# Optimization experiments

Measured on AMD Instinct MI355X. Metric: run time of the kernel, lower is better.

Reference implementation:

```python
import jax, jax.numpy as jnp
import numpy as np

SHIFT = 7  # shift_size; pad = 3


def _gn(x, w, b, eps=1e-5):
    # GroupNorm(1, C): normalize over (C,H,W) per sample, affine per channel
    m = jnp.mean(x, axis=(1, 2, 3), keepdims=True)
    v = jnp.var(x, axis=(1, 2, 3), keepdims=True)
    return (x - m) * jax.lax.rsqrt(v + eps) * w[None, :, None, None] + b[None, :, None, None]


def _conv1x1(x, w, b):
    return jnp.einsum('bchw,oc->bohw', x, w) + b[None, :, None, None]


def _gelu(x):
    return jax.nn.gelu(x, approximate=False)


def _shift_h(x, size):
    # CUDA kernel semantics: g = c // ceil(C/size); s = -(g - size//2);
    # out[n,c,h,w] = x[n,c,h+s,w] if in-bounds else 0  (dim=2)
    B, C, H, W = x.shape
    pad = size // 2
    group = -(-C // size)  # ceil
    s = pad - (jnp.arange(C) // group)              # [C], values in [-pad, pad]
    xp = jnp.pad(x, ((0, 0), (0, 0), (pad, pad), (0, 0)))
    idx = jnp.arange(H)[None, :] + s[:, None] + pad  # [C,H], in [0, H+2p-1]
    c = jnp.arange(C)[:, None]
    return xp[:, c, idx, :]


def _shift_w(x, size):
    return _shift_h(x.swapaxes(2, 3), size).swapaxes(2, 3)


def _axial_shift(x, c1w, c1b, n1w, n1b, c21w, c21b, c22w, c22b, n2w, n2b, c3w, c3b):
    x = _gelu(_gn(_conv1x1(x, c1w, c1b), n1w, n1b))
    x_lr = _shift_w(x, SHIFT)
    x_td = _shift_h(x, SHIFT)
    x_lr = _gelu(_conv1x1(x_lr, c21w, c21b))
    x_td = _gelu(_conv1x1(x_td, c22w, c22b))
    x = _gn(x_lr + x_td, n2w, n2b)
    return _conv1x1(x, c3w, c3b)


def setup_inputs() -> dict:
    B, C, H, W = 16, 256, 56, 56
    HID = 4 * C
    key = jax.random.key(0)
    ks = jax.random.split(key, 8)
    wscale = 0.05
    inp = {
        'x': jax.random.normal(ks[0], (B, C, H, W), jnp.float32),
        'n1_w': jnp.ones((C,), jnp.float32), 'n1_b': jnp.zeros((C,), jnp.float32),
        'as_c1_w': jax.random.normal(ks[1], (C, C), jnp.float32) * wscale,
        'as_c1_b': jnp.zeros((C,), jnp.float32),
        'as_n1_w': jnp.ones((C,), jnp.float32), 'as_n1_b': jnp.zeros((C,), jnp.float32),
        'as_c21_w': jax.random.normal(ks[2], (C, C), jnp.float32) * wscale,
        'as_c21_b': jnp.zeros((C,), jnp.float32),
        'as_c22_w': jax.random.normal(ks[3], (C, C), jnp.float32) * wscale,
        'as_c22_b': jnp.zeros((C,), jnp.float32),
        'as_n2_w': jnp.ones((C,), jnp.float32), 'as_n2_b': jnp.zeros((C,), jnp.float32),
        'as_c3_w': jax.random.normal(ks[4], (C, C), jnp.float32) * wscale,
        'as_c3_b': jnp.zeros((C,), jnp.float32),
        'n2_w': jnp.ones((C,), jnp.float32), 'n2_b': jnp.zeros((C,), jnp.float32),
        'fc1_w': jax.random.normal(ks[5], (HID, C), jnp.float32) * wscale,
        'fc1_b': jnp.zeros((HID,), jnp.float32),
        'fc2_w': jax.random.normal(ks[6], (C, HID), jnp.float32) * wscale,
        'fc2_b': jnp.zeros((C,), jnp.float32),
    }
    return inp


def reference(x, n1_w, n1_b, as_c1_w, as_c1_b, as_n1_w, as_n1_b,
              as_c21_w, as_c21_b, as_c22_w, as_c22_b, as_n2_w, as_n2_b,
              as_c3_w, as_c3_b, n2_w, n2_b, fc1_w, fc1_b, fc2_w, fc2_b):
    # AxialShiftedBlock: x = x + AxialShift(norm1(x)); x = x + Mlp(norm2(x))
    h = _gn(x, n1_w, n1_b)
    h = _axial_shift(h, as_c1_w, as_c1_b, as_n1_w, as_n1_b,
                     as_c21_w, as_c21_b, as_c22_w, as_c22_b,
                     as_n2_w, as_n2_b, as_c3_w, as_c3_b)
    x = x + h
    h = _gn(x, n2_w, n2_b)
    h = _gelu(_conv1x1(h, fc1_w, fc1_b))
    h = _conv1x1(h, fc2_w, fc2_b)
    return x + h
```

## Files before the change

kernel.cpp:

```cpp
#include <hip/hip_runtime.h>

typedef __attribute__((ext_vector_type(4))) float f32x4;
typedef __attribute__((ext_vector_type(8))) short bf16x8;
typedef __attribute__((ext_vector_type(4))) unsigned short u16x4;
typedef unsigned short u16;

#define HW 3136
#define NSEG 49
#define NELF 802816.0f
#define EPS 1e-5f

__device__ __forceinline__ short f2bf(float f) {
  union { float f; unsigned u; } v; v.f = f;
  unsigned r = (v.u + 0x7FFFu + ((v.u >> 16) & 1u)) >> 16;
  return (short)r;
}
__device__ __forceinline__ float b2f(u16 u) {
  union { unsigned u; float f; } v; v.u = ((unsigned)u) << 16;
  return v.f;
}
__device__ __forceinline__ float fgelu(float x) {
  float x2 = x * x;
  float u = x * (0.7978845608f + 0.0356774081f * x2);
  float e = __expf(-2.0f * u);
  return x * __builtin_amdgcn_rcpf(1.0f + e);
}
__device__ __forceinline__ void gload16(const void* g, void* l) {
  __builtin_amdgcn_global_load_lds(
      (const __attribute__((address_space(1))) void*)(uintptr_t)g,
      (__attribute__((address_space(3))) void*)(unsigned)(uintptr_t)l,
      16, 0, 0);
}

__global__ void wfold_kernel(const float* __restrict__ c1, const float* __restrict__ c21,
                             const float* __restrict__ c22, const float* __restrict__ c3,
                             const float* __restrict__ fc1, const float* __restrict__ fc2,
                             const float* __restrict__ n1w, const float* __restrict__ an2w,
                             const float* __restrict__ n2w, u16* __restrict__ out) {
  int i = (blockIdx.x * 256 + threadIdx.x) * 4;
  const float* src; int off; const float* scale = nullptr;
  if (i < 65536)       { src = c1;  off = 0;       scale = n1w; }
  else if (i < 131072) { src = c21; off = 65536; }
  else if (i < 196608) { src = c22; off = 131072; }
  else if (i < 262144) { src = c3;  off = 196608;  scale = an2w; }
  else if (i < 524288) { src = fc1; off = 262144;  scale = n2w; }
  else                 { src = fc2; off = 524288; }
  int li = i - off;
  float4 v = *(const float4*)(src + li);
  if (scale) {
    float4 g = *(const float4*)(scale + (li & 255));
    v.x *= g.x; v.y *= g.y; v.z *= g.z; v.w *= g.w;
  }
  u16x4 o4; o4[0] = (u16)f2bf(v.x); o4[1] = (u16)f2bf(v.y); o4[2] = (u16)f2bf(v.z); o4[3] = (u16)f2bf(v.w);
  *(u16x4*)(out + i) = o4;
}

__global__ void rowsum_kernel(const float* __restrict__ c1w, const float* __restrict__ c1b,
                              const float* __restrict__ n1w, const float* __restrict__ n1b,
                              const float* __restrict__ c3w, const float* __restrict__ c3b,
                              const float* __restrict__ an2w, const float* __restrict__ an2b,
                              const float* __restrict__ fc1w, const float* __restrict__ fc1b,
                              const float* __restrict__ n2w, const float* __restrict__ n2b,
                              float* __restrict__ sums) {
  int o = blockIdx.x * 256 + threadIdx.x;
  const float *W, *gw, *gb, *cb; float *Sg, *Sb; int row;
  if (o < 256)      { W = c1w;  gw = n1w;  gb = n1b;  cb = c1b;  Sg = sums;        Sb = sums + 256;  row = o; }
  else if (o < 512) { W = c3w;  gw = an2w; gb = an2b; cb = c3b;  Sg = sums + 512;  Sb = sums + 768;  row = o - 256; }
  else              { W = fc1w; gw = n2w;  gb = n2b;  cb = fc1b; Sg = sums + 1024; Sb = sums + 2048; row = o - 512; }
  float sg = 0.f, sb = 0.f;
  for (int c = 0; c < 256; c += 4) {
    float4 w = *(const float4*)(W + (size_t)row * 256 + c);
    float4 g = *(const float4*)(gw + c);
    float4 b = *(const float4*)(gb + c);
    sg += w.x * g.x + w.y * g.y + w.z * g.z + w.w * g.w;
    sb += w.x * b.x + w.y * b.y + w.z * b.z + w.w * b.w;
  }
  Sg[row] = sg; Sb[row] = sb + cb[row];
}

__global__ __launch_bounds__(256) void t0_kernel(const float* __restrict__ x,
                                                 u16* __restrict__ xT, float* __restrict__ st) {
  __shared__ __align__(16) u16 tile[64 * 256];
  const int t = threadIdx.x;
  const int n = blockIdx.x / NSEG;
  const int hw0 = (blockIdx.x % NSEG) * 64;
  const int pix = t & 63;
  float s = 0.f, q = 0.f;
#pragma unroll
  for (int r = 0; r < 16; ++r) {
    int cq = (t >> 6) + (r << 2);
    int c = cq * 4;
    u16x4 o4;
#pragma unroll
    for (int i = 0; i < 4; ++i) {
      float v = x[((size_t)n * 256 + c + i) * HW + hw0 + pix];
      s += v; q += v * v;
      o4[i] = (u16)f2bf(v);
    }
    int u = cq ^ ((pix & 15) << 2);
    *(u16x4*)((char*)tile + pix * 512 + u * 8) = o4;
  }
  __syncthreads();
  {
    const int p2 = t >> 2;
#pragma unroll
    for (int r = 0; r < 8; ++r) {
      int oct = (t & 3) + (r << 2);
      int up = (2 * oct) ^ ((p2 & 15) << 2);
      bf16x8 v = *(const bf16x8*)((char*)tile + p2 * 512 + up * 8);
      *(bf16x8*)&xT[((size_t)n * HW + hw0 + p2) * 256 + oct * 8] = v;
    }
  }
  __syncthreads();
  float* red = (float*)tile;
  red[t] = s; red[256 + t] = q;
  __syncthreads();
  for (int off = 128; off > 0; off >>= 1) {
    if (t < off) { red[t] += red[t + off]; red[256 + t] += red[256 + t + off]; }
    __syncthreads();
  }
  if (t == 0) { atomicAdd(&st[n * 2], red[0]); atomicAdd(&st[n * 2 + 1], red[256]); }
}

__global__ void e2_kernel(const u16* __restrict__ y, u16* __restrict__ tb,
                          const float* __restrict__ gw, const float* __restrict__ gb,
                          const float* __restrict__ stats) {
  const size_t NG = (size_t)16 * HW * 32;
  for (size_t g = (size_t)blockIdx.x * blockDim.x + threadIdx.x; g < NG;
       g += (size_t)gridDim.x * blockDim.x) {
    size_t base = g * 8;
    int n = (int)(base / 802816);
    int c0 = (int)(base & 255);
    float sm = stats[n * 2], sq = stats[n * 2 + 1];
    float mn = sm * (1.0f / NELF);
    float rstd = rsqrtf(sq * (1.0f / NELF) - mn * mn + EPS);
    bf16x8 v = *(const bf16x8*)(y + base);
    bf16x8 o;
#pragma unroll
    for (int j = 0; j < 8; ++j) {
      float sc = rstd * gw[c0 + j];
      float sh = gb[c0 + j] - mn * sc;
      o[j] = f2bf(fgelu(b2f((u16)v[j]) * sc + sh));
    }
    *(bf16x8*)(tb + base) = o;
  }
}

template<int EPI>
__global__ __launch_bounds__(512, 2) void gemmW2(
    const u16* __restrict__ actT, const u16* __restrict__ wt,
    const float* __restrict__ Sg, const float* __restrict__ Sb,
    const float* __restrict__ stats_in, float* __restrict__ stats_out,
    const u16* __restrict__ residCL, u16* __restrict__ outT)
{
  __shared__ __align__(16) u16 lds[79872];
  const int t = threadIdx.x;
  const int lane = t & 63, wave = t >> 6;
  const int fr = lane & 15, fq = lane >> 4;
  const int wo = wave >> 1, wp = wave & 1;
  const int n = blockIdx.x / 14;
  const int hw0 = (blockIdx.x % 14) * 224;
  const size_t nHW = (size_t)n * HW;

  {
    int u0 = t, u1 = t + 512;
    int r0 = u0 >> 2, sg0 = ((u0 & 3) - (r0 >> 1)) & 3;
    int r1 = u1 >> 2, sg1 = ((u1 & 3) - (r1 >> 1)) & 3;
    const u16* w0 = wt + (size_t)r0 * 256 + sg0 * 8;
    const u16* w1 = wt + (size_t)r1 * 256 + sg1 * 8;
#pragma unroll
    for (int k = 0; k < 8; ++k) {
      gload16(w0 + k * 32, &lds[k * 8192 + wave * 512]);
      gload16(w1 + k * 32, &lds[k * 8192 + 4096 + wave * 512]);
    }
  }

  int aU[4];
#pragma unroll
  for (int os = 0; os < 4; ++os) { int row = wo * 64 + os * 16 + fr; aU[os] = (4 * row + ((fq + (row >> 1)) & 3)) * 8; }
  int bO[7];
#pragma unroll
  for (int ps = 0; ps < 7; ++ps) {
    int pix = wp * 112 + ps * 16 + fr;
    bO[ps] = (pix * 4 + (fq ^ (pix & 3))) * 8;
  }

  const u16* srcB0; const u16* srcB1;
  {
    int v0 = wave * 128 + lane, v1 = v0 + 64;
    int p0 = v0 >> 2, j0 = (v0 & 3) ^ (p0 & 3);
    int p1 = v1 >> 2, j1 = (v1 & 3) ^ (p1 & 3);
    srcB0 = actT + (nHW + hw0 + p0) * 256 + j0 * 8;
    srcB1 = actT + (nHW + hw0 + p1) * 256 + j1 * 8;
  }
  auto stageB = [&](int par, int ks) {
    if (wave < 7) {
      gload16(srcB0 + ks * 32, &lds[65536 + par * 7168 + (wave * 128) * 8]);
      gload16(srcB1 + ks * 32, &lds[65536 + par * 7168 + (wave * 128 + 64) * 8]);
    }
  };

  f32x4 acc[4][7];
#pragma unroll
  for (int a = 0; a < 4; ++a)
#pragma unroll
    for (int b = 0; b < 7; ++b) acc[a][b] = (f32x4){0.f, 0.f, 0.f, 0.f};

  stageB(0, 0);
  __syncthreads();

#pragma unroll
  for (int k = 0; k < 8; ++k) {
    if (k < 7) stageB((k + 1) & 1, k + 1);
    bf16x8 afr[4], bfr[7];
#pragma unroll
    for (int os = 0; os < 4; ++os) afr[os] = *(const bf16x8*)&lds[k * 8192 + aU[os]];
#pragma unroll
    for (int ps = 0; ps < 7; ++ps) bfr[ps] = *(const bf16x8*)&lds[65536 + (k & 1) * 7168 + bO[ps]];
#pragma unroll
    for (int os = 0; os < 4; ++os)
#pragma unroll
      for (int ps = 0; ps < 7; ++ps)
        acc[os][ps] = __builtin_amdgcn_mfma_f32_16x16x32_bf16(afr[os], bfr[ps], acc[os][ps], 0, 0, 0);
    __syncthreads();
  }

  char* tl = (char*)lds;
  float sm = stats_in[n * 2], sq = stats_in[n * 2 + 1];
  float mn = sm * (1.0f / NELF);
  float rstd = rsqrtf(sq * (1.0f / NELF) - mn * mn + EPS);
  float mr = mn * rstd;
  float lsum = 0.f, lsq = 0.f;
#pragma unroll
  for (int os = 0; os < 4; ++os) {
    const int ob = wo * 64 + os * 16 + fq * 4;
    float4 g4 = *(const float4*)&Sg[ob];
    float4 s4 = *(const float4*)&Sb[ob];
    float be[4] = {s4.x - mr * g4.x, s4.y - mr * g4.y, s4.z - mr * g4.z, s4.w - mr * g4.w};
#pragma unroll
    for (int ps = 0; ps < 7; ++ps) {
      const int pix = wp * 112 + ps * 16 + fr;
      u16x4 rv = {0, 0, 0, 0};
      if (EPI == 1) rv = *(const u16x4*)&residCL[(nHW + hw0 + pix) * 256 + ob];
      u16x4 pk;
#pragma unroll
      for (int j = 0; j < 4; ++j) {
        float v = fmaf(acc[os][ps][j], rstd, be[j]);
        if (EPI == 1) v += b2f(rv[j]);
        lsum += v; lsq += v * v;
        pk[j] = (u16)f2bf(v);
      }
      const int qd = wo * 16 + os * 4 + fq;
      const int uq = qd ^ ((pix & 15) << 2);
      *(u16x4*)(tl + pix * 512 + uq * 8) = pk;
    }
  }
  __syncthreads();
#pragma unroll
  for (int r = 0; r < 14; ++r) {
    int idx = t + r * 512;
    int pix = idx >> 5, oct = idx & 31;
    int up = (2 * oct) ^ ((pix & 15) << 2);
    bf16x8 v = *(const bf16x8*)(tl + pix * 512 + up * 8);
    *(bf16x8*)&outT[(nHW + hw0 + pix) * 256 + oct * 8] = v;
  }
  __syncthreads();
  float* red = (float*)lds;
  red[t] = lsum; red[512 + t] = lsq;
  __syncthreads();
  for (int off = 256; off > 0; off >>= 1) {
    if (t < off) { red[t] += red[t + off]; red[512 + t] += red[512 + t + off]; }
    __syncthreads();
  }
  if (t == 0) { atomicAdd(&stats_out[n * 2], red[0]); atomicAdd(&stats_out[n * 2 + 1], red[512]); }
}

__global__ __launch_bounds__(512, 2) void gemm_dual4(
    const u16* __restrict__ tT, const u16* __restrict__ w21, const u16* __restrict__ w22,
    const float* __restrict__ b21, const float* __restrict__ b22,
    float* __restrict__ stats_out, u16* __restrict__ zT)
{
  __shared__ __align__(16) u16 lds[47616];
  const int t = threadIdx.x;
  const int lane = t & 63, wave = t >> 6;
  const int fr = lane & 15, fq = lane >> 4;
  const int n = blockIdx.x / 28;
  const int hw0 = (blockIdx.x % 28) * 112;
  const size_t nHW = (size_t)n * HW;

  const int u = (t < 448) ? t : 447;
  const int jl = u / 112, p = u - jl * 112;
  const int pix = hw0 + p;
  const int wc = pix % 56, hc = pix / 56;

  bf16x8 gA0, gA1, gB0, gB1;
  auto gatherIssue = [&](int ks) {
    int c0 = ks * 32 + jl * 8;
    int g0 = c0 / 37;
    int s0 = 3 - g0;
    int pa0 = pix + s0;           pa0 = pa0 < 0 ? 0 : (pa0 > HW - 1 ? HW - 1 : pa0);
    int pa1 = pix + s0 - 1;       pa1 = pa1 < 0 ? 0 : (pa1 > HW - 1 ? HW - 1 : pa1);
    int pb0 = pix + 56 * s0;      pb0 = pb0 < 0 ? 0 : (pb0 > HW - 1 ? HW - 1 : pb0);
    int pb1 = pix + 56 * (s0 - 1); pb1 = pb1 < 0 ? 0 : (pb1 > HW - 1 ? HW - 1 : pb1);
    gA0 = *(const bf16x8*)(tT + (nHW + pa0) * 256 + c0);
    gA1 = *(const bf16x8*)(tT + (nHW + pa1) * 256 + c0);
    gB0 = *(const bf16x8*)(tT + (nHW + pb0) * 256 + c0);
    gB1 = *(const bf16x8*)(tT + (nHW + pb1) * 256 + c0);
  };
  auto gatherWrite = [&](int par, int ks) {
    int c0 = ks * 32 + jl * 8;
    int g0 = c0 / 37;
    int s0 = 3 - g0;
    int js = (g0 + 1) * 37 - c0; if (js > 8) js = 8;
    bool a0 = (unsigned)(wc + s0) < 56u, a1 = (unsigned)(wc + s0 - 1) < 56u;
    bool b0 = (unsigned)(hc + s0) < 56u, b1 = (unsigned)(hc + s0 - 1) < 56u;
    bf16x8 va, vb;
#pragma unroll
    for (int j = 0; j < 8; ++j) {
      bool lo = j < js;
      va[j] = lo ? (a0 ? gA0[j] : (short)0) : (a1 ? gA1[j] : (short)0);
      vb[j] = lo ? (b0 ? gB0[j] : (short)0) : (b1 ? gB1[j] : (short)0);
    }
    if (t < 448) {
      *(bf16x8*)&lds[32768 + par * 3712 + (jl * 116 + p) * 8] = va;
      *(bf16x8*)&lds[40192 + par * 3712 + (jl * 116 + p) * 8] = vb;
    }
  };
  auto stageW = [&](int par, int ks) {
    int u0 = t; int r0 = u0 >> 2, sg0 = ((u0 & 3) - (r0 >> 1)) & 3;
    int u1 = t + 512; int r1 = u1 >> 2, sg1 = ((u1 & 3) - (r1 >> 1)) & 3;
    gload16(w21 + (size_t)r0 * 256 + ks * 32 + sg0 * 8, &lds[par * 8192 + wave * 512]);
    gload16(w21 + (size_t)r1 * 256 + ks * 32 + sg1 * 8, &lds[par * 8192 + 4096 + wave * 512]);
    gload16(w22 + (size_t)r0 * 256 + ks * 32 + sg0 * 8, &lds[16384 + par * 8192 + wave * 512]);
    gload16(w22 + (size_t)r1 * 256 + ks * 32 + sg1 * 8, &lds[16384 + par * 8192 + 4096 + wave * 512]);
  };

  int aU[2], bP[7];
#pragma unroll
  for (int os = 0; os < 2; ++os) { int row = wave * 32 + os * 16 + fr; aU[os] = (4 * row + ((fq + (row >> 1)) & 3)) * 8; }
#pragma unroll
  for (int ps = 0; ps < 7; ++ps) bP[ps] = (fq * 116 + ps * 16 + fr) * 8;

  f32x4 accA[2][7], accB[2][7];
#pragma unroll
  for (int a = 0; a < 2; ++a)
#pragma unroll
    for (int b = 0; b < 7; ++b) { accA[a][b] = (f32x4){0, 0, 0, 0}; accB[a][b] = (f32x4){0, 0, 0, 0}; }

  gatherIssue(0);
  stageW(0, 0);
  gatherWrite(0, 0);
  gatherIssue(1);
  __syncthreads();

#pragma unroll
  for (int k = 0; k < 8; ++k) {
    if (k < 7) stageW((k + 1) & 1, k + 1);
    bf16x8 afA[2], afB[2], bfA[7], bfB[7];
#pragma unroll
    for (int os = 0; os < 2; ++os) {
      afA[os] = *(const bf16x8*)&lds[(k & 1) * 8192 + aU[os]];
      afB[os] = *(const bf16x8*)&lds[16384 + (k & 1) * 8192 + aU[os]];
    }
#pragma unroll
    for (int ps = 0; ps < 7; ++ps) {
      bfA[ps] = *(const bf16x8*)&lds[32768 + (k & 1) * 3712 + bP[ps]];
      bfB[ps] = *(const bf16x8*)&lds[40192 + (k & 1) * 3712 + bP[ps]];
    }
#pragma unroll
    for (int os = 0; os < 2; ++os)
#pragma unroll
      for (int ps = 0; ps < 7; ++ps) {
        accA[os][ps] = __builtin_amdgcn_mfma_f32_16x16x32_bf16(afA[os], bfA[ps], accA[os][ps], 0, 0, 0);
        accB[os][ps] = __builtin_amdgcn_mfma_f32_16x16x32_bf16(afB[os], bfB[ps], accB[os][ps], 0, 0, 0);
      }
    if (k < 7) {
      gatherWrite((k + 1) & 1, k + 1);
      if (k < 6) gatherIssue(k + 2);
    }
    __syncthreads();
  }

  char* tl = (char*)lds;
  float lsum = 0.f, lsq = 0.f;
#pragma unroll
  for (int os = 0; os < 2; ++os) {
    const int ob = wave * 32 + os * 16 + fq * 4;
    float4 a4 = *(const float4*)&b21[ob];
    float4 c4 = *(const float4*)&b22[ob];
    float ba[4] = {a4.x, a4.y, a4.z, a4.w};
    float bb[4] = {c4.x, c4.y, c4.z, c4.w};
#pragma unroll
    for (int ps = 0; ps < 7; ++ps) {
      const int pixL = ps * 16 + fr;
      u16x4 pk;
#pragma unroll
      for (int j = 0; j < 4; ++j) {
        float z = fgelu(accA[os][ps][j] + ba[j]) + fgelu(accB[os][ps][j] + bb[j]);
        lsum += z; lsq += z * z;
        pk[j] = (u16)f2bf(z);
      }
      const int qd = wave * 8 + os * 4 + fq;
      const int uq = qd ^ ((pixL & 15) << 2);
      *(u16x4*)(tl + pixL * 512 + uq * 8) = pk;
    }
  }
  __syncthreads();
#pragma unroll
  for (int r = 0; r < 7; ++r) {
    int idx = t + r * 512;
    int pixL = idx >> 5, oct = idx & 31;
    int up = (2 * oct) ^ ((pixL & 15) << 2);
    bf16x8 v = *(const bf16x8*)(tl + pixL * 512 + up * 8);
    *(bf16x8*)&zT[(nHW + hw0 + pixL) * 256 + oct * 8] = v;
  }
  __syncthreads();
  float* red = (float*)lds;
  red[t] = lsum; red[512 + t] = lsq;
  __syncthreads();
  for (int off = 256; off > 0; off >>= 1) {
    if (t < off) { red[t] += red[t + off]; red[512 + t] += red[512 + t + off]; }
    __syncthreads();
  }
  if (t == 0) { atomicAdd(&stats_out[n * 2], red[0]); atomicAdd(&stats_out[n * 2 + 1], red[512]); }
}

__global__ __launch_bounds__(512, 2) void gemm_mlp(
    const u16* __restrict__ x2T, const u16* __restrict__ wfc1, const u16* __restrict__ wfc2,
    const float* __restrict__ Sg, const float* __restrict__ Sb, const float* __restrict__ bias2,
    const float* __restrict__ stats_in, float* __restrict__ out_f32)
{
  __shared__ __align__(16) u16 lds[75008];
  const int t = threadIdx.x;
  const int lane = t & 63, wave = t >> 6;
  const int fr = lane & 15, fq = lane >> 4;
  const int n = blockIdx.x / 28;
  const int hw0 = (blockIdx.x % 28) * 112;
  const size_t nHW = (size_t)n * HW;

  auto stageWm = [&](int par, int s) {
    int chunk = s >> 4, kk = s & 7;
    int u0 = t; int r0 = u0 >> 2, sg0 = ((u0 & 3) - (r0 >> 1)) & 3;
    int u1 = t + 512; int r1 = u1 >> 2, sg1 = ((u1 & 3) - (r1 >> 1)) & 3;
    if (((s >> 3) & 1) == 0) {
      gload16(wfc1 + (size_t)(chunk * 256 + r0) * 256 + kk * 32 + sg0 * 8, &lds[par * 8192 + wave * 512]);
      gload16(wfc1 + (size_t)(chunk * 256 + r1) * 256 + kk * 32 + sg1 * 8, &lds[par * 8192 + 4096 + wave * 512]);
    } else {
      gload16(wfc2 + (size_t)r0 * 1024 + chunk * 256 + kk * 32 + sg0 * 8, &lds[par * 8192 + wave * 512]);
      gload16(wfc2 + (size_t)r1 * 1024 + chunk * 256 + kk * 32 + sg1 * 8, &lds[par * 8192 + 4096 + wave * 512]);
    }
  };

#pragma unroll
  for (int i = 0; i < 7; ++i) {
    int u = wave * 448 + i * 64 + lane;
    int j = u / 112, p = u - j * 112;
    bf16x8 v = *(const bf16x8*)(x2T + (nHW + hw0 + p) * 256 + j * 8);
    *(bf16x8*)&lds[16384 + (j * 113 + p) * 8] = v;
  }
  stageWm(0, 0);

  float sm = stats_in[n * 2], sq = stats_in[n * 2 + 1];
  float mn = sm * (1.0f / NELF);
  float rstd = rsqrtf(sq * (1.0f / NELF) - mn * mn + EPS);
  float mr = mn * rstd;

  int aU[2];
#pragma unroll
  for (int os = 0; os < 2; ++os) { int row = wave * 32 + os * 16 + fr; aU[os] = (4 * row + ((fq + (row >> 1)) & 3)) * 8; }

  f32x4 hacc[2][7], oacc[2][7];
#pragma unroll
  for (int a = 0; a < 2; ++a)
#pragma unroll
    for (int b = 0; b < 7; ++b) { hacc[a][b] = (f32x4){0, 0, 0, 0}; oacc[a][b] = (f32x4){0, 0, 0, 0}; }

  __syncthreads();

  for (int s = 0; s < 64; ++s) {
    if (s < 63) stageWm((s + 1) & 1, s + 1);
    const int kk = s & 7;
    const bool bph = (s >> 3) & 1;
    bf16x8 afr[2], bfr[7];
#pragma unroll
    for (int os = 0; os < 2; ++os) afr[os] = *(const bf16x8*)&lds[(s & 1) * 8192 + aU[os]];
    if (!bph) {
#pragma unroll
      for (int ps = 0; ps < 7; ++ps)
        bfr[ps] = *(const bf16x8*)&lds[16384 + ((kk * 4 + fq) * 113 + ps * 16 + fr) * 8];
#pragma unroll
      for (int os = 0; os < 2; ++os)
#pragma unroll
        for (int ps = 0; ps < 7; ++ps)
          hacc[os][ps] = __builtin_amdgcn_mfma_f32_16x16x32_bf16(afr[os], bfr[ps], hacc[os][ps], 0, 0, 0);
    } else {
#pragma unroll
      for (int ps = 0; ps < 7; ++ps)
        bfr[ps] = *(const bf16x8*)&lds[45312 + ((kk * 4 + fq) * 116 + ps * 16 + fr) * 8];
#pragma unroll
      for (int os = 0; os < 2; ++os)
#pragma unroll
        for (int ps = 0; ps < 7; ++ps)
          oacc[os][ps] = __builtin_amdgcn_mfma_f32_16x16x32_bf16(afr[os], bfr[ps], oacc[os][ps], 0, 0, 0);
    }
    if ((s & 15) == 7) {
      const int hcb = (s >> 4) * 256;
#pragma unroll
      for (int os = 0; os < 2; ++os) {
        const int hcl = wave * 32 + os * 16 + fq * 4;
        const int hc = hcb + hcl;
        float4 g4 = *(const float4*)&Sg[hc];
        float4 s4 = *(const float4*)&Sb[hc];
        float be[4] = {s4.x - mr * g4.x, s4.y - mr * g4.y, s4.z - mr * g4.z, s4.w - mr * g4.w};
        const int jH = hcl >> 3;
#pragma unroll
        for (int ps = 0; ps < 7; ++ps) {
          const int pixL = ps * 16 + fr;
          u16x4 pk;
#pragma unroll
          for (int j = 0; j < 4; ++j)
            pk[j] = (u16)f2bf(fgelu(fmaf(hacc[os][ps][j], rstd, be[j])));
          *(u16x4*)&lds[45312 + (jH * 116 + pixL) * 8 + (fq & 1) * 4] = pk;
          hacc[os][ps] = (f32x4){0, 0, 0, 0};
        }
      }
    }
    __syncthreads();
  }

#pragma unroll
  for (int os = 0; os < 2; ++os) {
    const int ob = wave * 32 + os * 16 + fq * 4;
    float4 b4 = *(const float4*)&bias2[ob];
    float bb[4] = {b4.x, b4.y, b4.z, b4.w};
#pragma unroll
    for (int ps = 0; ps < 7; ++ps) {
      const int pixL = ps * 16 + fr;
      u16x4 rv = *(const u16x4*)&lds[16384 + ((ob >> 3) * 113 + pixL) * 8 + (ob & 4)];
#pragma unroll
      for (int j = 0; j < 4; ++j) {
        float v = oacc[os][ps][j] + bb[j] + b2f(rv[j]);
        out_f32[((size_t)n * 256 + ob + j) * HW + hw0 + pixL] = v;
      }
    }
  }
}

extern "C" void kernel_launch(void* const* d_in, const int* in_sizes, int n_in,
                              void* d_out, int out_size, void* d_ws, size_t ws_size,
                              hipStream_t stream) {
  const float* x     = (const float*)d_in[0];
  const float* n1_w  = (const float*)d_in[1];
  const float* n1_b  = (const float*)d_in[2];
  const float* c1_w  = (const float*)d_in[3];
  const float* c1_b  = (const float*)d_in[4];
  const float* an1_w = (const float*)d_in[5];
  const float* an1_b = (const float*)d_in[6];
  const float* c21_w = (const float*)d_in[7];
  const float* c21_b = (const float*)d_in[8];
  const float* c22_w = (const float*)d_in[9];
  const float* c22_b = (const float*)d_in[10];
  const float* an2_w = (const float*)d_in[11];
  const float* an2_b = (const float*)d_in[12];
  const float* c3_w  = (const float*)d_in[13];
  const float* c3_b  = (const float*)d_in[14];
  const float* n2_w  = (const float*)d_in[15];
  const float* n2_b  = (const float*)d_in[16];
  const float* fc1_w = (const float*)d_in[17];
  const float* fc1_b = (const float*)d_in[18];
  const float* fc2_w = (const float*)d_in[19];
  const float* fc2_b = (const float*)d_in[20];

  char* ws = (char*)d_ws;
  float* stats = (float*)ws;
  float* sums  = (float*)(ws + 1024);
  u16* wbuf = (u16*)(ws + 16384);
  u16* wb_c1g  = wbuf;
  u16* wb_c21  = wbuf + 65536;
  u16* wb_c22  = wbuf + 131072;
  u16* wb_c3g  = wbuf + 196608;
  u16* wb_fc1g = wbuf + 262144;
  u16* wb_fc2  = wbuf + 524288;
  const size_t AB = 25690112;
  char* A0 = ws + 1638400;
  u16* xT  = (u16*)(A0);
  u16* yT  = (u16*)(A0 + AB);
  u16* tT  = (u16*)(A0 + 2 * AB);
  u16* zT  = (u16*)(A0 + 3 * AB);
  u16* x2T = (u16*)(A0 + 4 * AB);
  float* out = (float*)d_out;

  hipMemsetAsync(stats, 0, 512, stream);
  wfold_kernel<<<768, 256, 0, stream>>>(c1_w, c21_w, c22_w, c3_w, fc1_w, fc2_w,
                                        n1_w, an2_w, n2_w, wbuf);
  rowsum_kernel<<<6, 256, 0, stream>>>(c1_w, c1_b, n1_w, n1_b, c3_w, c3_b, an2_w, an2_b,
                                       fc1_w, fc1_b, n2_w, n2_b, sums);
  t0_kernel<<<784, 256, 0, stream>>>(x, xT, stats + 0);
  gemmW2<0><<<224, 512, 0, stream>>>(xT, wb_c1g, sums, sums + 256,
                                     stats + 0, stats + 32, nullptr, yT);
  e2_kernel<<<2048, 256, 0, stream>>>(yT, tT, an1_w, an1_b, stats + 32);
  gemm_dual4<<<448, 512, 0, stream>>>(tT, wb_c21, wb_c22, c21_b, c22_b, stats + 64, zT);
  gemmW2<1><<<224, 512, 0, stream>>>(zT, wb_c3g, sums + 512, sums + 768,
                                     stats + 64, stats + 96, xT, x2T);
  gemm_mlp<<<448, 512, 0, stream>>>(x2T, wb_fc1g, wb_fc2, sums + 1024, sums + 2048,
                                    fc2_b, stats + 96, out);
}
```

Baseline: 282.9 us.

## Load MLP weight fragments directly from global memory instead of LDS staging

The fused fc1/fc2 MLP kernel no longer stages weight tiles into double-buffered LDS with async loads. Each wave now reads its A fragments straight from global (L2-resident) memory into registers. The k-loop is reorganised into four hidden chunks, each doing a full fc1 pass, GELU write-back to LDS, then an fc2 pass, which cuts barriers from one per k-step to two per chunk. This removes LDS traffic and synchronisation and shrinks the LDS footprint. In exchange, global load latency is exposed to the MFMA loop and each wave issues redundant weight fetches.

```diff
diff --git a/kernel.cpp b/kernel.cpp
--- a/kernel.cpp
+++ b/kernel.cpp
@@ -425,86 +425,70 @@
   if (t == 0) { atomicAdd(&stats_out[n * 2], red[0]); atomicAdd(&stats_out[n * 2 + 1], red[512]); }
 }
 
-__global__ __launch_bounds__(512, 2) void gemm_mlp(
+__global__ __launch_bounds__(512, 2) void mlp3(
     const u16* __restrict__ x2T, const u16* __restrict__ wfc1, const u16* __restrict__ wfc2,
     const float* __restrict__ Sg, const float* __restrict__ Sb, const float* __restrict__ bias2,
     const float* __restrict__ stats_in, float* __restrict__ out_f32)
 {
-  __shared__ __align__(16) u16 lds[75008];
+  __shared__ __align__(16) u16 lds[58624];
   const int t = threadIdx.x;
   const int lane = t & 63, wave = t >> 6;
   const int fr = lane & 15, fq = lane >> 4;
   const int n = blockIdx.x / 28;
   const int hw0 = (blockIdx.x % 28) * 112;
   const size_t nHW = (size_t)n * HW;
-
-  auto stageWm = [&](int par, int s) {
-    int chunk = s >> 4, kk = s & 7;
-    int u0 = t; int r0 = u0 >> 2, sg0 = ((u0 & 3) - (r0 >> 1)) & 3;
-    int u1 = t + 512; int r1 = u1 >> 2, sg1 = ((u1 & 3) - (r1 >> 1)) & 3;
-    if (((s >> 3) & 1) == 0) {
-      gload16(wfc1 + (size_t)(chunk * 256 + r0) * 256 + kk * 32 + sg0 * 8, &lds[par * 8192 + wave * 512]);
-      gload16(wfc1 + (size_t)(chunk * 256 + r1) * 256 + kk * 32 + sg1 * 8, &lds[par * 8192 + 4096 + wave * 512]);
-    } else {
-      gload16(wfc2 + (size_t)r0 * 1024 + chunk * 256 + kk * 32 + sg0 * 8, &lds[par * 8192 + wave * 512]);
-      gload16(wfc2 + (size_t)r1 * 1024 + chunk * 256 + kk * 32 + sg1 * 8, &lds[par * 8192 + 4096 + wave * 512]);
-    }
-  };
+  const int HOFF = 28928;
 
 #pragma unroll
   for (int i = 0; i < 7; ++i) {
     int u = wave * 448 + i * 64 + lane;
     int j = u / 112, p = u - j * 112;
     bf16x8 v = *(const bf16x8*)(x2T + (nHW + hw0 + p) * 256 + j * 8);
-    *(bf16x8*)&lds[16384 + (j * 113 + p) * 8] = v;
-  }
-  stageWm(0, 0);
+    *(bf16x8*)&lds[(j * 113 + p) * 8] = v;
+  }
 
   float sm = stats_in[n * 2], sq = stats_in[n * 2 + 1];
   float mn = sm * (1.0f / NELF);
   float rstd = rsqrtf(sq * (1.0f / NELF) - mn * mn + EPS);
   float mr = mn * rstd;
 
-  int aU[2];
-#pragma unroll
-  for (int os = 0; os < 2; ++os) { int row = wave * 32 + os * 16 + fr; aU[os] = (4 * row + ((fq + (row >> 1)) & 3)) * 8; }
-
-  f32x4 hacc[2][7], oacc[2][7];
+  const int arow = wave * 32 + fr;
+  const u16* w1base = wfc1 + (size_t)arow * 256 + fq * 8;
+  const u16* w2base = wfc2 + (size_t)arow * 1024 + fq * 8;
+
+  f32x4 oacc[2][7];
 #pragma unroll
   for (int a = 0; a < 2; ++a)
 #pragma unroll
-    for (int b = 0; b < 7; ++b) { hacc[a][b] = (f32x4){0, 0, 0, 0}; oacc[a][b] = (f32x4){0, 0, 0, 0}; }
-
-  __syncthreads();
-
-  for (int s = 0; s < 64; ++s) {
-    if (s < 63) stageWm((s + 1) & 1, s + 1);
-    const int kk = s & 7;
-    const bool bph = (s >> 3) & 1;
-    bf16x8 afr[2], bfr[7];
-#pragma unroll
-    for (int os = 0; os < 2; ++os) afr[os] = *(const bf16x8*)&lds[(s & 1) * 8192 + aU[os]];
-    if (!bph) {
+    for (int b = 0; b < 7; ++b) oacc[a][b] = (f32x4){0.f, 0.f, 0.f, 0.f};
+
+  __syncthreads();
+
+  for (int c = 0; c < 4; ++c) {
+    f32x4 hacc[2][7];
+#pragma unroll
+    for (int a = 0; a < 2; ++a)
+#pragma unroll
+      for (int b = 0; b < 7; ++b) hacc[a][b] = (f32x4){0.f, 0.f, 0.f, 0.f};
+
+    const u16* w1c = w1base + (size_t)c * 65536;
+#pragma unroll
+    for (int kk = 0; kk < 8; ++kk) {
+      bf16x8 a0 = *(const bf16x8*)(w1c + kk * 32);
+      bf16x8 a1 = *(const bf16x8*)(w1c + 4096 + kk * 32);
+      bf16x8 bfr[7];
 #pragma unroll
       for (int ps = 0; ps < 7; ++ps)
-        bfr[ps] = *(const bf16x8*)&lds[16384 + ((kk * 4 + fq) * 113 + ps * 16 + fr) * 8];
-#pragma unroll
-      for (int os = 0; os < 2; ++os)
-#pragma unroll
-        for (int ps = 0; ps < 7; ++ps)
-          hacc[os][ps] = __builtin_amdgcn_mfma_f32_16x16x32_bf16(afr[os], bfr[ps], hacc[os][ps], 0, 0, 0);
-    } else {
-#pragma unroll
-      for (int ps = 0; ps < 7; ++ps)
-        bfr[ps] = *(const bf16x8*)&lds[45312 + ((kk * 4 + fq) * 116 + ps * 16 + fr) * 8];
-#pragma unroll
-      for (int os = 0; os < 2; ++os)
-#pragma unroll
-        for (int ps = 0; ps < 7; ++ps)
-          oacc[os][ps] = __builtin_amdgcn_mfma_f32_16x16x32_bf16(afr[os], bfr[ps], oacc[os][ps], 0, 0, 0);
-    }
-    if ((s & 15) == 7) {
-      const int hcb = (s >> 4) * 256;
+        bfr[ps] = *(const bf16x8*)&lds[((kk * 4 + fq) * 113 + ps * 16 + fr) * 8];
+#pragma unroll
+      for (int ps = 0; ps < 7; ++ps) {
+        hacc[0][ps] = __builtin_amdgcn_mfma_f32_16x16x32_bf16(a0, bfr[ps], hacc[0][ps], 0, 0, 0);
+        hacc[1][ps] = __builtin_amdgcn_mfma_f32_16x16x32_bf16(a1, bfr[ps], hacc[1][ps], 0, 0, 0);
+      }
+    }
+
+    {
+      const int hcb = c * 256;
 #pragma unroll
       for (int os = 0; os < 2; ++os) {
         const int hcl = wave * 32 + os * 16 + fq * 4;
@@ -520,9 +504,25 @@
 #pragma unroll
           for (int j = 0; j < 4; ++j)
             pk[j] = (u16)f2bf(fgelu(fmaf(hacc[os][ps][j], rstd, be[j])));
-          *(u16x4*)&lds[45312 + (jH * 116 + pixL) * 8 + (fq & 1) * 4] = pk;
-          hacc[os][ps] = (f32x4){0, 0, 0, 0};
+          *(u16x4*)&lds[HOFF + (jH * 116 + pixL) * 8 + (fq & 1) * 4] = pk;
         }
+      }
+    }
+    __syncthreads();
+
+    const u16* w2c = w2base + c * 256;
+#pragma unroll
+    for (int kk = 0; kk < 8; ++kk) {
+      bf16x8 a0 = *(const bf16x8*)(w2c + kk * 32);
+      bf16x8 a1 = *(const bf16x8*)(w2c + 16384 + kk * 32);
+      bf16x8 bfr[7];
+#pragma unroll
+      for (int ps = 0; ps < 7; ++ps)
+        bfr[ps] = *(const bf16x8*)&lds[HOFF + ((kk * 4 + fq) * 116 + ps * 16 + fr) * 8];
+#pragma unroll
+      for (int ps = 0; ps < 7; ++ps) {
+        oacc[0][ps] = __builtin_amdgcn_mfma_f32_16x16x32_bf16(a0, bfr[ps], oacc[0][ps], 0, 0, 0);
+        oacc[1][ps] = __builtin_amdgcn_mfma_f32_16x16x32_bf16(a1, bfr[ps], oacc[1][ps], 0, 0, 0);
       }
     }
     __syncthreads();
@@ -536,7 +536,7 @@
 #pragma unroll
     for (int ps = 0; ps < 7; ++ps) {
       const int pixL = ps * 16 + fr;
-      u16x4 rv = *(const u16x4*)&lds[16384 + ((ob >> 3) * 113 + pixL) * 8 + (ob & 4)];
+      u16x4 rv = *(const u16x4*)&lds[((ob >> 3) * 113 + pixL) * 8 + (ob & 4)];
 #pragma unroll
       for (int j = 0; j < 4; ++j) {
         float v = oacc[os][ps][j] + bb[j] + b2f(rv[j]);
@@ -602,6 +602,6 @@
   gemm_dual4<<<448, 512, 0, stream>>>(tT, wb_c21, wb_c22, c21_b, c22_b, stats + 64, zT);
   gemmW2<1><<<224, 512, 0, stream>>>(zT, wb_c3g, sums + 512, sums + 768,
                                      stats + 64, stats + 96, xT, x2T);
-  gemm_mlp<<<448, 512, 0, stream>>>(x2T, wb_fc1g, wb_fc2, sums + 1024, sums + 2048,
-                                    fc2_b, stats + 96, out);
-}
+  mlp3<<<448, 512, 0, stream>>>(x2T, wb_fc1g, wb_fc2, sums + 1024, sums + 2048,
+                                fc2_b, stats + 96, out);
+}
```

After: 265.3 us (median of 2 runs). 1.07x faster.
